# Kernel optimization log

Measured on AMD Instinct MI355X. Metric: run time of the kernel, lower is better.

## Reference

```python
import jax, jax.numpy as jnp
import numpy as np

VOCAB_SIZE = 126
N_LABELS = VOCAB_SIZE + 2  # 128
START_IDX = N_LABELS - 2
STOP_IDX = N_LABELS - 1
NEG_INF = -10000.0


def setup_inputs() -> dict:
    key = jax.random.key(0)
    k1, k2, k3 = jax.random.split(key, 3)
    B, T = 512, 512
    logits = jax.random.normal(k1, (B, T, N_LABELS), dtype=jnp.float32)
    lens = jax.random.randint(k2, (B,), 1, T + 1, dtype=jnp.int64)
    transitions = jax.random.normal(k3, (N_LABELS, N_LABELS), dtype=jnp.float32)
    # CRF constraints from __init__: nothing transitions FROM start-as-target row,
    # nothing transitions INTO stop column (transitions[i, j] = score j -> i).
    transitions = transitions.at[START_IDX, :].set(NEG_INF)
    transitions = transitions.at[:, STOP_IDX].set(NEG_INF)
    return {"logits": logits, "lens": lens, "transitions": transitions}


def reference(logits, lens, transitions):
    """CRF forward algorithm (log partition function). Returns [B] norm."""
    B, T, n = logits.shape
    alpha0 = jnp.full((B, n), NEG_INF, dtype=logits.dtype).at[:, START_IDX].set(0.0)
    # mask[t, b] = 1 while t < lens[b] (matches c_lens > 0 per-step update)
    mask = (jnp.arange(T)[:, None] < lens[None, :]).astype(logits.dtype)  # [T, B]
    logits_t = jnp.transpose(logits, (1, 0, 2))  # [T, B, n]

    def step(alpha, inp):
        logit, m = inp  # [B, n], [B]
        # alpha_nxt[b, i] = logit[b, i] + logsumexp_j(trans[i, j] + alpha[b, j])
        alpha_nxt = jax.nn.logsumexp(transitions[None, :, :] + alpha[:, None, :], axis=2) + logit
        m = m[:, None]
        alpha = m * alpha_nxt + (1.0 - m) * alpha
        return alpha, None

    alpha, _ = jax.lax.scan(step, alpha0, (logits_t, mask))
    alpha = alpha + transitions[STOP_IDX][None, :]
    return jax.nn.logsumexp(alpha, axis=1)  # [B]
```

## Files before the change

kernel.cpp:

```cpp
#include <hip/hip_runtime.h>

#define NL 128
#define TT 512
#define NB 512
#define START_IDX 126
#define STOP_IDX 127

typedef __attribute__((ext_vector_type(8))) short bf16x8;
typedef __attribute__((ext_vector_type(4))) float f32x4;
typedef __attribute__((ext_vector_type(4))) unsigned u32x4;

__device__ __forceinline__ short f2bf(float x) {
    union { float f; unsigned u; } v; v.f = x;
    unsigned r = (v.u + 0x7FFFu + ((v.u >> 16) & 1u)) >> 16;
    return (short)r;
}

__device__ __forceinline__ unsigned cvt_pk_bf16(float lo, float hi) {
    unsigned r;
    asm("v_cvt_pk_bf16_f32 %0, %1, %2" : "=v"(r) : "v"(lo), "v"(hi));
    return r;
}

#define STEP(T_, PUB_, CONS_, EC_, EO_, RC_, RO_) do {                        \
    u32x4 bo_ = {bw0, bw1, bw2, bw3};                                         \
    bf16x8 bO_ = __builtin_bit_cast(bf16x8, bo_);                             \
    bf16x8 bA_ = __builtin_bit_cast(bf16x8, bvA);                             \
    bf16x8 bB_ = __builtin_bit_cast(bf16x8, bvB);                             \
    bf16x8 bC_ = __builtin_bit_cast(bf16x8, bvC);                             \
    f32x4 a0_ = {0.f,0.f,0.f,0.f}, a1_ = {0.f,0.f,0.f,0.f};                   \
    a0_ = __builtin_amdgcn_mfma_f32_16x16x32_bf16(afr[0][0], bO_, a0_, 0,0,0);\
    a1_ = __builtin_amdgcn_mfma_f32_16x16x32_bf16(afr[1][0], bO_, a1_, 0,0,0);\
    a0_ = __builtin_amdgcn_mfma_f32_16x16x32_bf16(afr[0][1], bA_, a0_, 0,0,0);\
    a1_ = __builtin_amdgcn_mfma_f32_16x16x32_bf16(afr[1][1], bA_, a1_, 0,0,0);\
    a0_ = __builtin_amdgcn_mfma_f32_16x16x32_bf16(afr[0][2], bB_, a0_, 0,0,0);\
    a1_ = __builtin_amdgcn_mfma_f32_16x16x32_bf16(afr[1][2], bB_, a1_, 0,0,0);\
    a0_ = __builtin_amdgcn_mfma_f32_16x16x32_bf16(afr[0][3], bC_, a0_, 0,0,0);\
    a1_ = __builtin_amdgcn_mfma_f32_16x16x32_bf16(afr[1][3], bC_, a1_, 0,0,0);\
    { int tp_ = (T_) + 2; if (tp_ > TT - 1) tp_ = TT - 1;                     \
      const float* lp_ = lsrc + (size_t)tp_ * NL;                             \
      RC_##0 = *(const f32x4*)(lp_ + eo0);                                    \
      RC_##1 = *(const f32x4*)(lp_ + eo1); }                                  \
    _Pragma("unroll")                                                         \
    for (int r_ = 0; r_ < 4; ++r_) {                                          \
        EO_##0[r_] = __expf(RO_##0[r_]);                                      \
        EO_##1[r_] = __expf(RO_##1[r_]);                                      \
    }                                                                         \
    float nv0_[4], nv1_[4];                                                   \
    _Pragma("unroll")                                                         \
    for (int r_ = 0; r_ < 4; ++r_) {                                          \
        nv0_[r_] = a0_[r_] * EC_##0[r_];                                      \
        nv1_[r_] = a1_[r_] * EC_##1[r_];                                      \
    }                                                                         \
    const bool live_ = (T_) < lenc;                                           \
    if (CONS_) {                                                              \
        float mx_ = fmaxf(fmaxf(smax[0][c], smax[1][c]),                      \
                          fmaxf(smax[2][c], smax[3][c]));                     \
        const unsigned eb_ = (__float_as_uint(mx_) >> 23) & 0xFFu;            \
        const float sc_ = __uint_as_float(((253u - eb_) & 0xFFu) << 23);      \
        _Pragma("unroll")                                                     \
        for (int r_ = 0; r_ < 4; ++r_) { nv0_[r_] *= sc_; nv1_[r_] *= sc_; }  \
        if (live_) cbi += (int)eb_ - 126;                                     \
    }                                                                         \
    if (PUB_) {                                                               \
        float lm_ = fmaxf(fmaxf(fmaxf(nv0_[0], nv0_[1]), fmaxf(nv0_[2], nv0_[3])), \
                          fmaxf(fmaxf(nv1_[0], nv1_[1]), fmaxf(nv1_[2], nv1_[3]))); \
        lm_ = fmaxf(lm_, __shfl_xor(lm_, 16));                                \
        lm_ = fmaxf(lm_, __shfl_xor(lm_, 32));                                \
        if (g == 0) smax[w][c] = lm_;                                         \
    }                                                                         \
    { const unsigned n0_ = cvt_pk_bf16(nv0_[0], nv0_[1]);                     \
      const unsigned n1_ = cvt_pk_bf16(nv0_[2], nv0_[3]);                     \
      const unsigned n2_ = cvt_pk_bf16(nv1_[0], nv1_[1]);                     \
      const unsigned n3_ = cvt_pk_bf16(nv1_[2], nv1_[3]);                     \
      bw0 = live_ ? n0_ : bw0;  bw1 = live_ ? n1_ : bw1;                      \
      bw2 = live_ ? n2_ : bw2;  bw3 = live_ ? n3_ : bw3; }                    \
    char* nb_ = sb[((T_) + 1) & 1];                                           \
    { u32x4 wv_ = {bw0, bw1, bw2, bw3};                                       \
      *(u32x4*)(nb_ + w * 1280 + slotOff) = wv_; }                            \
    __syncthreads();                                                          \
    bvA = *(const u32x4*)(nb_ + kA + slotOff);                                \
    bvB = *(const u32x4*)(nb_ + kB + slotOff);                                \
    bvC = *(const u32x4*)(nb_ + kC + slotOff);                                \
} while (0)

__global__ __launch_bounds__(256)
void crf_scan(const float* __restrict__ logits,
              const int* __restrict__ lens,
              const float* __restrict__ trans,
              float* __restrict__ out)
{
    const int b0   = blockIdx.x * 16;
    const int tid  = threadIdx.x;
    const int w    = tid >> 6;
    const int lane = tid & 63;
    const int c    = lane & 15;
    const int g    = lane >> 4;

    __shared__ __align__(16) char sb[2][4 * 16 * 80];
    __shared__ float smax[4][16];

    bf16x8 afr[2][4];
    #pragma unroll
    for (int mi = 0; mi < 2; ++mi) {
        const int M = w + 4 * mi;
        const float* rowp = trans + (M * 16 + c) * NL + 4 * g;
        #pragma unroll
        for (int pos = 0; pos < 4; ++pos) {
            const int kk = (w + pos) & 3;
            f32x4 lo4 = *(const f32x4*)(rowp + kk * 16);
            f32x4 hi4 = *(const f32x4*)(rowp + (kk + 4) * 16);
            bf16x8 a;
            #pragma unroll
            for (int j = 0; j < 4; ++j) {
                a[j]     = f2bf(__expf(lo4[j]));
                a[j + 4] = f2bf(__expf(hi4[j]));
            }
            afr[mi][pos] = a;
        }
    }

    int lenc = lens[b0 + c];
    lenc = lenc < 1 ? 1 : (lenc > TT ? TT : lenc);
    int gl = lenc;
    #pragma unroll
    for (int d = 1; d < 16; d <<= 1) { int o = __shfl_xor(gl, d); gl = gl > o ? gl : o; }
    const int glen = __builtin_amdgcn_readfirstlane(gl);

    const int slotOff = c * 80 + g * 16;
    const int kA = ((w + 1) & 3) * 1280;
    const int kB = ((w + 2) & 3) * 1280;
    const int kC = ((w + 3) & 3) * 1280;

    unsigned bw0 = 0u, bw1 = 0u, bw2 = 0u,
             bw3 = (w == 3 && g == 3) ? 0x00003F80u : 0u;
    { u32x4 z = {bw0, bw1, bw2, bw3};
      *(u32x4*)(sb[0] + w * 1280 + slotOff) = z; }
    __syncthreads();
    u32x4 bvA = *(const u32x4*)(sb[0] + kA + slotOff);
    u32x4 bvB = *(const u32x4*)(sb[0] + kB + slotOff);
    u32x4 bvC = *(const u32x4*)(sb[0] + kC + slotOff);

    const float* lsrc = logits + (size_t)(b0 + c) * TT * NL;
    const int eo0 = w * 16 + 4 * g;
    const int eo1 = (w + 4) * 16 + 4 * g;

    f32x4 R00, R01, R10, R11, E00, E01, E10, E11;
    R00 = *(const f32x4*)(lsrc + eo0);            R01 = *(const f32x4*)(lsrc + eo1);
    R10 = *(const f32x4*)(lsrc + NL + eo0);       R11 = *(const f32x4*)(lsrc + NL + eo1);
    #pragma unroll
    for (int r = 0; r < 4; ++r) {
        E00[r] = __expf(R00[r]); E01[r] = __expf(R01[r]);
        E10[r] = __expf(R10[r]); E11[r] = __expf(R11[r]);
    }

    int cbi = 0;
    int t = 0;
    for (; t + 4 <= glen; t += 4) {
        STEP(t + 0, false, false, E0, E1, R0, R1);
        STEP(t + 1, false, false, E1, E0, R1, R0);
        STEP(t + 2, true,  false, E0, E1, R0, R1);
        STEP(t + 3, false, true,  E1, E0, R1, R0);
    }
    for (; t < glen; ++t) {
        const bool pub = (t & 3) == 2, cons = (t & 3) == 3;
        if (t & 1) STEP(t, pub, cons, E1, E0, R1, R0);
        else       STEP(t, pub, cons, E0, E1, R0, R1);
    }

    if (w == 0) {
        float s = 0.f;
        const float* stopr = trans + STOP_IDX * NL + 4 * g;
        u32x4 grp[4];
        grp[0] = (u32x4){bw0, bw1, bw2, bw3};
        grp[1] = bvA; grp[2] = bvB; grp[3] = bvC;
        #pragma unroll
        for (int kk = 0; kk < 4; ++kk) {
            f32x4 t0 = *(const f32x4*)(stopr + kk * 16);
            f32x4 t1 = *(const f32x4*)(stopr + (kk + 4) * 16);
            #pragma unroll
            for (int i = 0; i < 2; ++i) {
                const unsigned wd = grp[kk][i];
                s += __uint_as_float(wd << 16)         * __expf(t0[2 * i]);
                s += __uint_as_float(wd & 0xFFFF0000u) * __expf(t0[2 * i + 1]);
            }
            #pragma unroll
            for (int i = 2; i < 4; ++i) {
                const unsigned wd = grp[kk][i];
                s += __uint_as_float(wd << 16)         * __expf(t1[2 * (i - 2)]);
                s += __uint_as_float(wd & 0xFFFF0000u) * __expf(t1[2 * (i - 2) + 1]);
            }
        }
        s += __shfl_xor(s, 16);
        s += __shfl_xor(s, 32);
        if (g == 0)
            out[b0 + c] = (float)cbi * 0.69314718055994531f + __logf(s);
    }
}

extern "C" void kernel_launch(void* const* d_in, const int* in_sizes, int n_in,
                              void* d_out, int out_size, void* d_ws, size_t ws_size,
                              hipStream_t stream) {
    const float* logits = (const float*)d_in[0];
    const int*   lens   = (const int*)d_in[1];
    const float* trans  = (const float*)d_in[2];
    float*       outp   = (float*)d_out;
    crf_scan<<<NB / 16, 256, 0, stream>>>(logits, lens, trans, outp);
}
```

Before: 177.8 us.

## Derive rescale max from exchanged bf16 alpha and use a lighter barrier

Drops the separate shared-memory max publish/consume path. Each thread now computes the column max over the alpha words it already holds, on the bf16 bit patterns, using unsigned integer max plus two shuffles. The global logit load is moved after the LDS store and the exp of the prefetched logits after the barrier, so that latency overlaps the sync. __syncthreads is replaced with an explicit lgkmcnt wait plus s_barrier, which avoids waiting on outstanding global loads. The tail loop no longer rescales, so a few steps may go unnormalized, and the integer max assumes all values are non-negative.

```diff
diff --git a/kernel.cpp b/kernel.cpp
--- a/kernel.cpp
+++ b/kernel.cpp
@@ -22,7 +22,14 @@
     return r;
 }
 
-#define STEP(T_, PUB_, CONS_, EC_, EO_, RC_, RO_) do {                        \
+__device__ __forceinline__ unsigned umx(unsigned a, unsigned b) { return a > b ? a : b; }
+
+#define BAR() do {                                                            \
+    asm volatile("s_waitcnt lgkmcnt(0)" ::: "memory");                        \
+    __builtin_amdgcn_s_barrier();                                             \
+} while (0)
+
+#define STEP(T_, RS_, EC_, EO_, RC_, RO_) do {                                \
     u32x4 bo_ = {bw0, bw1, bw2, bw3};                                         \
     bf16x8 bO_ = __builtin_bit_cast(bf16x8, bo_);                             \
     bf16x8 bA_ = __builtin_bit_cast(bf16x8, bvA);                             \
@@ -37,15 +44,6 @@
     a1_ = __builtin_amdgcn_mfma_f32_16x16x32_bf16(afr[1][2], bB_, a1_, 0,0,0);\
     a0_ = __builtin_amdgcn_mfma_f32_16x16x32_bf16(afr[0][3], bC_, a0_, 0,0,0);\
     a1_ = __builtin_amdgcn_mfma_f32_16x16x32_bf16(afr[1][3], bC_, a1_, 0,0,0);\
-    { int tp_ = (T_) + 2; if (tp_ > TT - 1) tp_ = TT - 1;                     \
-      const float* lp_ = lsrc + (size_t)tp_ * NL;                             \
-      RC_##0 = *(const f32x4*)(lp_ + eo0);                                    \
-      RC_##1 = *(const f32x4*)(lp_ + eo1); }                                  \
-    _Pragma("unroll")                                                         \
-    for (int r_ = 0; r_ < 4; ++r_) {                                          \
-        EO_##0[r_] = __expf(RO_##0[r_]);                                      \
-        EO_##1[r_] = __expf(RO_##1[r_]);                                      \
-    }                                                                         \
     float nv0_[4], nv1_[4];                                                   \
     _Pragma("unroll")                                                         \
     for (int r_ = 0; r_ < 4; ++r_) {                                          \
@@ -53,21 +51,24 @@
         nv1_[r_] = a1_[r_] * EC_##1[r_];                                      \
     }                                                                         \
     const bool live_ = (T_) < lenc;                                           \
-    if (CONS_) {                                                              \
-        float mx_ = fmaxf(fmaxf(smax[0][c], smax[1][c]),                      \
-                          fmaxf(smax[2][c], smax[3][c]));                     \
-        const unsigned eb_ = (__float_as_uint(mx_) >> 23) & 0xFFu;            \
+    if (RS_) {                                                                \
+        unsigned wl_[16] = {bw0, bw1, bw2, bw3,                               \
+                            bvA[0], bvA[1], bvA[2], bvA[3],                   \
+                            bvB[0], bvB[1], bvB[2], bvB[3],                   \
+                            bvC[0], bvC[1], bvC[2], bvC[3]};                  \
+        unsigned mx_ = 0u;                                                    \
+        _Pragma("unroll")                                                     \
+        for (int q_ = 0; q_ < 16; ++q_) {                                     \
+            mx_ = umx(mx_, wl_[q_] << 16);                                    \
+            mx_ = umx(mx_, wl_[q_] & 0xFFFF0000u);                            \
+        }                                                                     \
+        mx_ = umx(mx_, (unsigned)__shfl_xor((int)mx_, 16));                   \
+        mx_ = umx(mx_, (unsigned)__shfl_xor((int)mx_, 32));                   \
+        const unsigned eb_ = mx_ >> 23;                                       \
         const float sc_ = __uint_as_float(((253u - eb_) & 0xFFu) << 23);      \
         _Pragma("unroll")                                                     \
         for (int r_ = 0; r_ < 4; ++r_) { nv0_[r_] *= sc_; nv1_[r_] *= sc_; }  \
         if (live_) cbi += (int)eb_ - 126;                                     \
-    }                                                                         \
-    if (PUB_) {                                                               \
-        float lm_ = fmaxf(fmaxf(fmaxf(nv0_[0], nv0_[1]), fmaxf(nv0_[2], nv0_[3])), \
-                          fmaxf(fmaxf(nv1_[0], nv1_[1]), fmaxf(nv1_[2], nv1_[3]))); \
-        lm_ = fmaxf(lm_, __shfl_xor(lm_, 16));                                \
-        lm_ = fmaxf(lm_, __shfl_xor(lm_, 32));                                \
-        if (g == 0) smax[w][c] = lm_;                                         \
     }                                                                         \
     { const unsigned n0_ = cvt_pk_bf16(nv0_[0], nv0_[1]);                     \
       const unsigned n1_ = cvt_pk_bf16(nv0_[2], nv0_[3]);                     \
@@ -78,10 +79,19 @@
     char* nb_ = sb[((T_) + 1) & 1];                                           \
     { u32x4 wv_ = {bw0, bw1, bw2, bw3};                                       \
       *(u32x4*)(nb_ + w * 1280 + slotOff) = wv_; }                            \
-    __syncthreads();                                                          \
+    { int tp_ = (T_) + 2; if (tp_ > TT - 1) tp_ = TT - 1;                     \
+      const float* lp_ = lsrc + (size_t)tp_ * NL;                             \
+      RC_##0 = *(const f32x4*)(lp_ + eo0);                                    \
+      RC_##1 = *(const f32x4*)(lp_ + eo1); }                                  \
+    BAR();                                                                    \
     bvA = *(const u32x4*)(nb_ + kA + slotOff);                                \
     bvB = *(const u32x4*)(nb_ + kB + slotOff);                                \
     bvC = *(const u32x4*)(nb_ + kC + slotOff);                                \
+    _Pragma("unroll")                                                         \
+    for (int r_ = 0; r_ < 4; ++r_) {                                          \
+        EO_##0[r_] = __expf(RO_##0[r_]);                                      \
+        EO_##1[r_] = __expf(RO_##1[r_]);                                      \
+    }                                                                         \
 } while (0)
 
 __global__ __launch_bounds__(256)
@@ -98,7 +108,6 @@
     const int g    = lane >> 4;
 
     __shared__ __align__(16) char sb[2][4 * 16 * 80];
-    __shared__ float smax[4][16];
 
     bf16x8 afr[2][4];
     #pragma unroll
@@ -136,7 +145,7 @@
              bw3 = (w == 3 && g == 3) ? 0x00003F80u : 0u;
     { u32x4 z = {bw0, bw1, bw2, bw3};
       *(u32x4*)(sb[0] + w * 1280 + slotOff) = z; }
-    __syncthreads();
+    BAR();
     u32x4 bvA = *(const u32x4*)(sb[0] + kA + slotOff);
     u32x4 bvB = *(const u32x4*)(sb[0] + kB + slotOff);
     u32x4 bvC = *(const u32x4*)(sb[0] + kC + slotOff);
@@ -157,15 +166,14 @@
     int cbi = 0;
     int t = 0;
     for (; t + 4 <= glen; t += 4) {
-        STEP(t + 0, false, false, E0, E1, R0, R1);
-        STEP(t + 1, false, false, E1, E0, R1, R0);
-        STEP(t + 2, true,  false, E0, E1, R0, R1);
-        STEP(t + 3, false, true,  E1, E0, R1, R0);
+        STEP(t + 0, false, E0, E1, R0, R1);
+        STEP(t + 1, false, E1, E0, R1, R0);
+        STEP(t + 2, false, E0, E1, R0, R1);
+        STEP(t + 3, true,  E1, E0, R1, R0);
     }
     for (; t < glen; ++t) {
-        const bool pub = (t & 3) == 2, cons = (t & 3) == 3;
-        if (t & 1) STEP(t, pub, cons, E1, E0, R1, R0);
-        else       STEP(t, pub, cons, E0, E1, R0, R1);
+        if (t & 1) STEP(t, false, E1, E0, R1, R0);
+        else       STEP(t, false, E0, E1, R0, R1);
     }
 
     if (w == 0) {
```

Result: slower. 223.7 us (+25.8%).
